# Performance work log

Measured on AMD Instinct MI355X. Metric: run time of the kernel, lower is better.

Reference implementation:

```python
import jax, jax.numpy as jnp
import numpy as np

_LOG_2PI = float(np.log(2.0 * np.pi))
N = 4096
N_VARS = 128
N_SOURCES = 8
_EPS = 1e-6


def setup_inputs() -> dict:
    key = jax.random.key(0)
    ks = jax.random.split(key, 6)
    data = jax.random.normal(ks[0], (N, N_VARS), dtype=jnp.float32)
    sources = jax.random.randint(ks[1], (N,), 0, N_SOURCES, dtype=jnp.int32)
    miss_mask = jax.random.bernoulli(ks[2], 0.3, (N, N_VARS))
    # Strictly lower-triangular DAG weights, small spectral norm so I - W is well conditioned
    W_eff = jnp.tril(jax.random.normal(ks[3], (N_VARS, N_VARS), dtype=jnp.float32) * 0.05, k=-1)
    log_sigma2 = jnp.zeros((N_SOURCES, N_VARS), dtype=jnp.float32)
    mu = jnp.zeros((N_VARS,), dtype=jnp.float32)
    sample_weights = jax.random.uniform(ks[4], (N,), dtype=jnp.float32)
    return {"data": data, "W_eff": W_eff, "log_sigma2": log_sigma2, "mu": mu,
            "sample_weights": sample_weights, "sources": sources, "miss_mask": miss_mask}


def reference(data, W_eff, log_sigma2, mu, sample_weights, sources, miss_mask):
    # Gaussian log-likelihood over observed entries only, per sample.
    # Original torch code loops over unique (source, missingness-pattern) groups and
    # does a Cholesky of the observed sub-covariance Sigma_oo + eps*I.  We compute the
    # mathematically identical quantity fully batched via the masked-covariance trick:
    #   Sigma_tilde = M (Sigma + eps I) M + diag(1 - obs)
    # whose logdet equals logdet(Sigma_oo + eps I_oo) and whose quadratic form on the
    # zero-filled centred data equals x_o^T (Sigma_oo + eps I)^{-1} x_o.
    D = data.shape[1]
    I = jnp.eye(D, dtype=data.dtype)
    T = jnp.linalg.solve(I - W_eff, I)                       # [D, D]
    sigma2 = jnp.maximum(jnp.exp(log_sigma2), _EPS)          # [S, D]
    # Sigma_s = T^T diag(sigma2_s) T for every source
    Sigma = jnp.einsum('ij,si,ik->sjk', T, sigma2, T)        # [S, D, D]

    obs = (~miss_mask).astype(data.dtype)                    # [N, D]
    xc = (data - mu[None, :]) * obs                          # centred, zero at missing

    Sig_i = Sigma[sources] + _EPS * I                        # [N, D, D]
    M = obs[:, :, None] * obs[:, None, :]                    # [N, D, D] obs outer obs
    Sig_t = Sig_i * M + I * (1.0 - obs)[:, None, :]          # identity on missing coords

    L = jnp.linalg.cholesky(Sig_t)                           # [N, D, D]
    z = jax.scipy.linalg.solve_triangular(L, xc[:, :, None], lower=True)[:, :, 0]
    quad = jnp.sum(z * z, axis=1)                            # [N]
    logdet = 2.0 * jnp.sum(jnp.log(jnp.diagonal(L, axis1=1, axis2=2)), axis=1)
    d_obs = jnp.sum(obs, axis=1)                             # [N]
    ll = -0.5 * (quad + logdet + d_obs * _LOG_2PI)           # [N]
    return jnp.sum(ll * sample_weights)
```

## Files before the change

### kernel.cpp

```cpp
#include <hip/hip_runtime.h>
#include <math.h>

#define DD 128
#define NSRC 8
#define EMAX 32
#define MFAST 62
#define LOG_2PI 1.83787706640934548356f
#define LN2F 0.69314718055994531f
#define EPSF 1e-6f

__device__ inline int tri_row_of(int e) {
    float f = sqrtf(8.f * (float)e + 1.f);
    int r = (int)((f - 1.f) * 0.5f);
    if ((r + 1) * (r + 2) / 2 <= e) ++r;
    else if (r * (r + 1) / 2 > e) --r;
    return r;
}

__global__ __launch_bounds__(128) void k_precompute(
    const float* __restrict__ W, const float* __restrict__ ls2,
    const unsigned int* __restrict__ mw, int n_words,
    float* __restrict__ Q, float* __restrict__ ldS, int* __restrict__ flag)
{
    __shared__ float Bs[DD][DD + 1];
    __shared__ float r[4][DD + 1];
    __shared__ float sinv[DD];
    __shared__ float part2[2];
    const int tid = threadIdx.x;
    const int s   = blockIdx.x >> 5;
    const int i0  = (blockIdx.x & 31) * 4;

    int gid = (blockIdx.x * 128 + tid) * 4;
    int f = 0;
    #pragma unroll
    for (int t = 0; t < 4; ++t) {
        int idx = gid + t;
        if (idx < n_words) {
            unsigned int v = mw[idx];
            if (v > 1u) f |= 1;
            if (v == 0x3F800000u) f |= 2;
        }
    }
    unsigned long long bA = __ballot(f & 1);
    unsigned long long bB = __ballot(f & 2);
    if ((tid & 63) == 0) {
        int fw = (bA ? 1 : 0) | (bB ? 2 : 0);
        if (fw) atomicOr(flag, fw);
    }

    for (int idx = tid; idx < DD * DD; idx += 128) {
        int row = idx >> 7, col = idx & 127;
        Bs[row][col] = (row == col ? 1.f : 0.f) - W[idx];
    }
    sinv[tid] = 1.f / fmaxf(expf(ls2[s * DD + tid]), EPSF);
    __syncthreads();
    for (int a = 0; a < 4; ++a)
        r[a][tid] = Bs[i0 + a][tid] * sinv[tid];
    __syncthreads();

    const int j = tid;
    float acc0 = 0.f, acc1 = 0.f, acc2 = 0.f, acc3 = 0.f;
    #pragma unroll 4
    for (int d = 0; d < DD; ++d) {
        float bj = Bs[j][d];
        acc0 += r[0][d] * bj;
        acc1 += r[1][d] * bj;
        acc2 += r[2][d] * bj;
        acc3 += r[3][d] * bj;
    }
    size_t base = ((size_t)s * DD + i0) * DD + j;
    Q[base         ] = acc0;
    Q[base +     DD] = acc1;
    Q[base + 2 * DD] = acc2;
    Q[base + 3 * DD] = acc3;

    if (i0 == 0) {
        float v = logf(fmaxf(expf(ls2[s * DD + tid]), EPSF));
        for (int o = 32; o; o >>= 1) v += __shfl_down(v, o, 64);
        if ((tid & 63) == 0) part2[tid >> 6] = v;
        __syncthreads();
        if (tid == 0) ldS[s] = part2[0] + part2[1];
    }
}

__global__ __launch_bounds__(64) void k_fast(
    const float* __restrict__ data, const float* __restrict__ mu,
    const float* __restrict__ wgt, const int* __restrict__ src,
    const void* __restrict__ miss, const int* __restrict__ layoutFlag,
    const float* __restrict__ Q, const float* __restrict__ ldS,
    float* __restrict__ partial, int* __restrict__ ovf_count,
    int* __restrict__ ovf_list)
{
    __shared__ __align__(16) float xsh[DD];
    __shared__ float ysh[DD];
    __shared__ int   midx[DD];
    __shared__ float csc[2][64];

    const int i = blockIdx.x, lane = threadIdx.x;
    const int s = src[i];
    const float* Qs = Q + (size_t)s * DD * DD;
    const size_t base = (size_t)i * DD;

    const int f = *layoutFlag;
    bool mm0, mm1;
    if (f & 2) {
        mm0 = ((const float*)miss)[base + lane]      != 0.f;
        mm1 = ((const float*)miss)[base + lane + 64] != 0.f;
    } else if (f & 1) {
        mm0 = ((const unsigned char*)miss)[base + lane]      != 0;
        mm1 = ((const unsigned char*)miss)[base + lane + 64] != 0;
    } else {
        mm0 = ((const int*)miss)[base + lane]      != 0;
        mm1 = ((const int*)miss)[base + lane + 64] != 0;
    }

    unsigned long long b0 = __ballot(mm0), b1 = __ballot(mm1);
    const int m = __popcll(b0) + __popcll(b1);
    if (m > MFAST) {
        if (lane == 0) { int pos = atomicAdd(ovf_count, 1); ovf_list[pos] = i; }
        return;
    }
    unsigned long long lt = (1ull << lane) - 1ull;
    if (mm0) midx[__popcll(b0 & lt)] = lane;
    if (mm1) midx[__popcll(b0) + __popcll(b1 & lt)] = lane + 64;

    float xv0 = mm0 ? 0.f : (data[base + lane]      - mu[lane]);
    float xv1 = mm1 ? 0.f : (data[base + lane + 64] - mu[lane + 64]);
    xsh[lane] = xv0;
    xsh[lane + 64] = xv1;
    __syncthreads();

    const float4* q0 = (const float4*)(Qs + (size_t)lane * DD);
    const float4* q1 = (const float4*)(Qs + (size_t)(lane + 64) * DD);
    const float4* x4 = (const float4*)xsh;
    float a0 = 0.f, a1 = 0.f;
    #pragma unroll 8
    for (int d = 0; d < DD / 4; ++d) {
        float4 xx = x4[d];
        float4 qa = q0[d], qb = q1[d];
        a0 += qa.x * xx.x + qa.y * xx.y + qa.z * xx.z + qa.w * xx.w;
        a1 += qb.x * xx.x + qb.y * xx.y + qb.z * xx.z + qb.w * xx.w;
    }
    ysh[lane] = a0;
    ysh[lane + 64] = a1;
    float p = xv0 * a0 + xv1 * a1;
    for (int o = 32; o; o >>= 1) p += __shfl_down(p, o, 64);
    __syncthreads();

    const int cntT = ((m + 1) * (m + 2)) >> 1;
    unsigned key[EMAX];
    float    val[EMAX];
    #pragma unroll
    for (int t = 0; t < EMAX; ++t) {
        key[t] = 0u; val[t] = 0.f;
        int e = lane + (t << 6);
        if (e < cntT) {
            int q  = tri_row_of(e);
            int jc = m - q;
            int ir = jc + (e - ((q * (q + 1)) >> 1));
            float v;
            if (ir == m) {
                v = (jc == m) ? 0.f : ysh[midx[jc]];
            } else {
                v = Qs[(size_t)(midx[ir] * DD + midx[jc])];
            }
            key[t] = ((unsigned)jc << 8) | (unsigned)ir;
            val[t] = v;
            if (jc == 0) csc[0][ir] = v;
        }
    }
    __syncthreads();

    float logacc = 0.f;
    #pragma unroll 1
    for (int k = 0; k < m; ++k) {
        const int pb = k & 1;
        float dk = csc[pb][k];
        float invd = __builtin_amdgcn_rcpf(dk);
        logacc += __log2f(dk);
        const unsigned boundA = (unsigned)(k + 1) << 8;
        const unsigned boundB = (unsigned)(k + 2) << 8;
        #pragma unroll
        for (int t = 0; t < EMAX; ++t) {
            bool alive = (key[t] >= boundA);
            if (!__any(alive)) break;
            if (alive) {
                int ir = (int)(key[t] & 255u);
                int jc = (int)(key[t] >> 8);
                float ci = csc[pb][ir];
                float cj = csc[pb][jc];
                val[t] -= ci * cj * invd;
                if (key[t] < boundB) csc[pb ^ 1][ir] = val[t];
            }
        }
        __syncthreads();
    }

    if (lane == 0) {
        float ll = -0.5f * ((p + val[0]) + logacc * LN2F + ldS[s]
                            + (float)(DD - m) * LOG_2PI);
        atomicAdd(&partial[i & 63], ll * wgt[i]);
    }
}

__global__ __launch_bounds__(128) void k_fallback(
    const float* __restrict__ data, const float* __restrict__ mu,
    const float* __restrict__ wgt, const int* __restrict__ src,
    const void* __restrict__ miss, const int* __restrict__ layoutFlag,
    const float* __restrict__ Q, const float* __restrict__ ldS,
    float* __restrict__ partial, const int* __restrict__ ovf_count,
    const int* __restrict__ ovf_list)
{
    __shared__ __align__(16) float xsh[DD];
    __shared__ float ysh[DD];
    __shared__ int   midx[DD];
    __shared__ float cscv[DD + 1];
    __shared__ float tri[(DD + 1) * (DD + 2) / 2];
    __shared__ float bc[2];
    __shared__ float red[2];
    __shared__ int   sh_m;

    const int tid = threadIdx.x;
    for (int j = blockIdx.x; j < *ovf_count; j += gridDim.x) {
        const int i = ovf_list[j];
        if (tid == 0) sh_m = 0;
        __syncthreads();

        const int s = src[i];
        const float* Qs = Q + (size_t)s * DD * DD;
        const int f = *layoutFlag;
        const size_t g = (size_t)i * DD + tid;
        bool mm;
        if (f & 2)      mm = ((const float*)miss)[g] != 0.f;
        else if (f & 1) mm = ((const unsigned char*)miss)[g] != 0;
        else            mm = ((const int*)miss)[g] != 0;

        float xv = mm ? 0.f : (data[g] - mu[tid]);
        xsh[tid] = xv;
        if (mm) { int pos = atomicAdd(&sh_m, 1); midx[pos] = tid; }
        __syncthreads();
        const int m = sh_m;

        const float4* qrow = (const float4*)(Qs + (size_t)tid * DD);
        const float4* x4   = (const float4*)xsh;
        float acc = 0.f;
        #pragma unroll 8
        for (int d = 0; d < DD / 4; ++d) {
            float4 q = qrow[d], xx = x4[d];
            acc += q.x * xx.x + q.y * xx.y + q.z * xx.z + q.w * xx.w;
        }
        ysh[tid] = acc;
        float pp = xv * acc;
        for (int o = 32; o; o >>= 1) pp += __shfl_down(pp, o, 64);
        if ((tid & 63) == 0) red[tid >> 6] = pp;
        __syncthreads();

        const int cntA = (m * (m + 1)) >> 1;
        for (int e = tid; e < cntA; e += 128) {
            int a = tri_row_of(e);
            int b = e - ((a * (a + 1)) >> 1);
            tri[e] = Qs[(size_t)midx[a] * DD + midx[b]];
        }
        for (int b = tid; b < m; b += 128) tri[cntA + b] = ysh[midx[b]];
        if (tid == 0) tri[cntA + m] = 0.f;
        __syncthreads();

        float logacc = 0.f;
        if (m > 0) {
            if (tid == 0) {
                float d0 = tri[0];
                bc[1] = d0;
                float sq = sqrtf(d0);
                bc[0] = 1.f / sq;
                tri[0] = sq;
            }
            __syncthreads();
            for (int k = 0; k < m; ++k) {
                float inv = bc[0];
                if (tid == 0) logacc += logf(bc[1]);
                for (int ii = k + 1 + tid; ii <= m; ii += 128) {
                    int off = (ii * (ii + 1)) >> 1;
                    float v = tri[off + k] * inv;
                    tri[off + k] = v;
                    cscv[ii] = v;
                }
                __syncthreads();
                int qn  = m - k;
                int cnt = (qn * (qn + 1)) >> 1;
                for (int e = tid; e < cnt; e += 128) {
                    int ri = tri_row_of(e);
                    int rj = e - ((ri * (ri + 1)) >> 1);
                    int ii = k + 1 + ri, jj = k + 1 + rj;
                    int off = (ii * (ii + 1)) >> 1;
                    float v = tri[off + jj] - cscv[ii] * cscv[jj];
                    if (ii == jj && jj == k + 1 && k + 1 < m) {
                        bc[1] = v;
                        float sq = sqrtf(v);
                        bc[0] = 1.f / sq;
                        tri[off + jj] = sq;
                    } else {
                        tri[off + jj] = v;
                    }
                }
                __syncthreads();
            }
        }

        if (tid == 0) {
            float quad2 = (m > 0) ? -tri[cntA + m] : 0.f;
            float quad1 = red[0] + red[1];
            float ll = -0.5f * ((quad1 - quad2) + logacc + ldS[s]
                                + (float)(DD - m) * LOG_2PI);
            atomicAdd(&partial[i & 63], ll * wgt[i]);
        }
        __syncthreads();
    }
}

__global__ __launch_bounds__(64) void k_reduce(
    const float* __restrict__ partial, float* __restrict__ out)
{
    int l = threadIdx.x;
    float v = partial[l];
    for (int o = 32; o; o >>= 1) v += __shfl_down(v, o, 64);
    if (l == 0) out[0] = v;
}

extern "C" void kernel_launch(void* const* d_in, const int* in_sizes, int n_in,
                              void* d_out, int out_size, void* d_ws, size_t ws_size,
                              hipStream_t stream)
{
    const float* data = (const float*)d_in[0];
    const float* W    = (const float*)d_in[1];
    const float* ls2  = (const float*)d_in[2];
    const float* mu   = (const float*)d_in[3];
    const float* wgt  = (const float*)d_in[4];
    const int*   src  = (const int*)d_in[5];
    const void*  miss = (const void*)d_in[6];
    float* out = (float*)d_out;

    float* Q        = (float*)d_ws;
    float* ldS      = Q + (size_t)NSRC * DD * DD;
    float* partial  = ldS + NSRC;
    int*   flag     = (int*)(partial + 64);
    int*   ovf_cnt  = flag + 1;
    int*   ovf_list = flag + 2;

    const int n       = in_sizes[0] / DD;
    const int n_words = (n * DD) / 4;

    hipMemsetAsync(partial, 0, 66 * sizeof(float), stream);
    hipLaunchKernelGGL(k_precompute, dim3(NSRC * 32), dim3(128), 0, stream,
                       W, ls2, (const unsigned int*)miss, n_words, Q, ldS, flag);
    hipLaunchKernelGGL(k_fast, dim3(n), dim3(64), 0, stream,
                       data, mu, wgt, src, miss, flag, Q, ldS,
                       partial, ovf_cnt, ovf_list);
    hipLaunchKernelGGL(k_fallback, dim3(64), dim3(128), 0, stream,
                       data, mu, wgt, src, miss, flag, Q, ldS,
                       partial, ovf_cnt, ovf_list);
    hipLaunchKernelGGL(k_reduce, dim3(1), dim3(64), 0, stream, partial, out);
}
```

Baseline: 180.1 us.

## Pack four samples per block in fast kernel and fuse fallback with final reduce

The fast kernel now handles four samples per 256-thread block, one wavefront each, and keeps overflow samples in the block with m forced to zero so block-wide barriers stay uniform. The elimination loop runs to the largest m among the four wavefronts, so every wavefront waits at each __syncthreads for the slowest one. The fallback and reduce kernels are merged into a single one-block tail kernel, which removes one launch but makes any overflow samples run serially.

Result: slower. 210.5 us (+16.9%).

```diff
diff --git a/kernel.cpp b/kernel.cpp
--- a/kernel.cpp
+++ b/kernel.cpp
@@ -5,6 +5,7 @@
 #define NSRC 8
 #define EMAX 32
 #define MFAST 62
+#define WPB 4
 #define LOG_2PI 1.83787706640934548356f
 #define LN2F 0.69314718055994531f
 #define EPSF 1e-6f
@@ -83,7 +84,7 @@
     }
 }
 
-__global__ __launch_bounds__(64) void k_fast(
+__global__ __launch_bounds__(256) void k_fast(
     const float* __restrict__ data, const float* __restrict__ mu,
     const float* __restrict__ wgt, const int* __restrict__ src,
     const void* __restrict__ miss, const int* __restrict__ layoutFlag,
@@ -91,13 +92,16 @@
     float* __restrict__ partial, int* __restrict__ ovf_count,
     int* __restrict__ ovf_list)
 {
-    __shared__ __align__(16) float xsh[DD];
-    __shared__ float ysh[DD];
-    __shared__ int   midx[DD];
-    __shared__ float csc[2][64];
-
-    const int i = blockIdx.x, lane = threadIdx.x;
-    const int s = src[i];
+    __shared__ __align__(16) float xsh[WPB][DD];
+    __shared__ float ysh[WPB][DD];
+    __shared__ int   midx[WPB][64];
+    __shared__ float csc[WPB][2][64];
+    __shared__ int   msh[WPB];
+
+    const int w    = threadIdx.x >> 6;
+    const int lane = threadIdx.x & 63;
+    const int i    = blockIdx.x * WPB + w;
+    const int s    = src[i];
     const float* Qs = Q + (size_t)s * DD * DD;
     const size_t base = (size_t)i * DD;
 
@@ -115,24 +119,27 @@
     }
 
     unsigned long long b0 = __ballot(mm0), b1 = __ballot(mm1);
-    const int m = __popcll(b0) + __popcll(b1);
-    if (m > MFAST) {
-        if (lane == 0) { int pos = atomicAdd(ovf_count, 1); ovf_list[pos] = i; }
-        return;
-    }
+    const int m_real = __popcll(b0) + __popcll(b1);
+    const bool skip = (m_real > MFAST);
+    if (skip && lane == 0) { int pos = atomicAdd(ovf_count, 1); ovf_list[pos] = i; }
+    const int m = skip ? 0 : m_real;
+    if (lane == 0) msh[w] = m;
+
     unsigned long long lt = (1ull << lane) - 1ull;
-    if (mm0) midx[__popcll(b0 & lt)] = lane;
-    if (mm1) midx[__popcll(b0) + __popcll(b1 & lt)] = lane + 64;
+    if (!skip) {
+        if (mm0) midx[w][__popcll(b0 & lt)] = lane;
+        if (mm1) midx[w][__popcll(b0) + __popcll(b1 & lt)] = lane + 64;
+    }
 
     float xv0 = mm0 ? 0.f : (data[base + lane]      - mu[lane]);
     float xv1 = mm1 ? 0.f : (data[base + lane + 64] - mu[lane + 64]);
-    xsh[lane] = xv0;
-    xsh[lane + 64] = xv1;
+    xsh[w][lane] = xv0;
+    xsh[w][lane + 64] = xv1;
     __syncthreads();
 
     const float4* q0 = (const float4*)(Qs + (size_t)lane * DD);
     const float4* q1 = (const float4*)(Qs + (size_t)(lane + 64) * DD);
-    const float4* x4 = (const float4*)xsh;
+    const float4* x4 = (const float4*)xsh[w];
     float a0 = 0.f, a1 = 0.f;
     #pragma unroll 8
     for (int d = 0; d < DD / 4; ++d) {
@@ -141,11 +148,13 @@
         a0 += qa.x * xx.x + qa.y * xx.y + qa.z * xx.z + qa.w * xx.w;
         a1 += qb.x * xx.x + qb.y * xx.y + qb.z * xx.z + qb.w * xx.w;
     }
-    ysh[lane] = a0;
-    ysh[lane + 64] = a1;
+    ysh[w][lane] = a0;
+    ysh[w][lane + 64] = a1;
     float p = xv0 * a0 + xv1 * a1;
     for (int o = 32; o; o >>= 1) p += __shfl_down(p, o, 64);
     __syncthreads();
+
+    const int kmax = max(max(msh[0], msh[1]), max(msh[2], msh[3]));
 
     const int cntT = ((m + 1) * (m + 2)) >> 1;
     unsigned key[EMAX];
@@ -160,56 +169,58 @@
             int ir = jc + (e - ((q * (q + 1)) >> 1));
             float v;
             if (ir == m) {
-                v = (jc == m) ? 0.f : ysh[midx[jc]];
+                v = (jc == m) ? 0.f : ysh[w][midx[w][jc]];
             } else {
-                v = Qs[(size_t)(midx[ir] * DD + midx[jc])];
+                v = Qs[(size_t)(midx[w][ir] * DD + midx[w][jc])];
             }
             key[t] = ((unsigned)jc << 8) | (unsigned)ir;
             val[t] = v;
-            if (jc == 0) csc[0][ir] = v;
+            if (jc == 0) csc[w][0][ir] = v;
         }
     }
     __syncthreads();
 
     float logacc = 0.f;
     #pragma unroll 1
-    for (int k = 0; k < m; ++k) {
-        const int pb = k & 1;
-        float dk = csc[pb][k];
-        float invd = __builtin_amdgcn_rcpf(dk);
-        logacc += __log2f(dk);
-        const unsigned boundA = (unsigned)(k + 1) << 8;
-        const unsigned boundB = (unsigned)(k + 2) << 8;
-        #pragma unroll
-        for (int t = 0; t < EMAX; ++t) {
-            bool alive = (key[t] >= boundA);
-            if (!__any(alive)) break;
-            if (alive) {
-                int ir = (int)(key[t] & 255u);
-                int jc = (int)(key[t] >> 8);
-                float ci = csc[pb][ir];
-                float cj = csc[pb][jc];
-                val[t] -= ci * cj * invd;
-                if (key[t] < boundB) csc[pb ^ 1][ir] = val[t];
+    for (int k = 0; k < kmax; ++k) {
+        if (k < m) {
+            const int pb = k & 1;
+            float dk = csc[w][pb][k];
+            float invd = __builtin_amdgcn_rcpf(dk);
+            logacc += __log2f(dk);
+            const unsigned boundA = (unsigned)(k + 1) << 8;
+            const unsigned boundB = (unsigned)(k + 2) << 8;
+            #pragma unroll
+            for (int t = 0; t < EMAX; ++t) {
+                bool alive = (key[t] >= boundA);
+                if (!__any(alive)) break;
+                if (alive) {
+                    int ir = (int)(key[t] & 255u);
+                    int jc = (int)(key[t] >> 8);
+                    float ci = csc[w][pb][ir];
+                    float cj = csc[w][pb][jc];
+                    val[t] -= ci * cj * invd;
+                    if (key[t] < boundB) csc[w][pb ^ 1][ir] = val[t];
+                }
             }
         }
         __syncthreads();
     }
 
-    if (lane == 0) {
+    if (lane == 0 && !skip) {
         float ll = -0.5f * ((p + val[0]) + logacc * LN2F + ldS[s]
                             + (float)(DD - m) * LOG_2PI);
         atomicAdd(&partial[i & 63], ll * wgt[i]);
     }
 }
 
-__global__ __launch_bounds__(128) void k_fallback(
+__global__ __launch_bounds__(128) void k_tail(
     const float* __restrict__ data, const float* __restrict__ mu,
     const float* __restrict__ wgt, const int* __restrict__ src,
     const void* __restrict__ miss, const int* __restrict__ layoutFlag,
     const float* __restrict__ Q, const float* __restrict__ ldS,
     float* __restrict__ partial, const int* __restrict__ ovf_count,
-    const int* __restrict__ ovf_list)
+    const int* __restrict__ ovf_list, float* __restrict__ out)
 {
     __shared__ __align__(16) float xsh[DD];
     __shared__ float ysh[DD];
@@ -221,7 +232,8 @@
     __shared__ int   sh_m;
 
     const int tid = threadIdx.x;
-    for (int j = blockIdx.x; j < *ovf_count; j += gridDim.x) {
+    const int novf = *ovf_count;
+    for (int j = 0; j < novf; ++j) {
         const int i = ovf_list[j];
         if (tid == 0) sh_m = 0;
         __syncthreads();
@@ -315,15 +327,13 @@
         }
         __syncthreads();
     }
-}
-
-__global__ __launch_bounds__(64) void k_reduce(
-    const float* __restrict__ partial, float* __restrict__ out)
-{
-    int l = threadIdx.x;
-    float v = partial[l];
-    for (int o = 32; o; o >>= 1) v += __shfl_down(v, o, 64);
-    if (l == 0) out[0] = v;
+
+    __syncthreads();
+    if (tid < 64) {
+        float v = partial[tid];
+        for (int o = 32; o; o >>= 1) v += __shfl_down(v, o, 64);
+        if (tid == 0) out[0] = v;
+    }
 }
 
 extern "C" void kernel_launch(void* const* d_in, const int* in_sizes, int n_in,
@@ -352,11 +362,10 @@
     hipMemsetAsync(partial, 0, 66 * sizeof(float), stream);
     hipLaunchKernelGGL(k_precompute, dim3(NSRC * 32), dim3(128), 0, stream,
                        W, ls2, (const unsigned int*)miss, n_words, Q, ldS, flag);
-    hipLaunchKernelGGL(k_fast, dim3(n), dim3(64), 0, stream,
+    hipLaunchKernelGGL(k_fast, dim3(n / WPB), dim3(64 * WPB), 0, stream,
                        data, mu, wgt, src, miss, flag, Q, ldS,
                        partial, ovf_cnt, ovf_list);
-    hipLaunchKernelGGL(k_fallback, dim3(64), dim3(128), 0, stream,
+    hipLaunchKernelGGL(k_tail, dim3(1), dim3(128), 0, stream,
                        data, mu, wgt, src, miss, flag, Q, ldS,
-                       partial, ovf_cnt, ovf_list);
-    hipLaunchKernelGGL(k_reduce, dim3(1), dim3(64), 0, stream, partial, out);
-}
+                       partial, ovf_cnt, ovf_list, out);
+}
```

## Coalesce Q matvec and gather, skip missing rows, merge tail kernels

Applied to the files above, without the earlier changes.

Reorganizes the fast-path matvec so each lane owns two adjacent output columns and streams rows of Q coalesced, skipping rows where the centred data is zero. The missing-index sub-block of Q is gathered once into a shared triangular buffer before the per-lane register fill. The fallback and final reduction kernels are merged into a single one-block kernel to drop a launch. This adds shared memory per block, which may lower occupancy, and serializes overflow samples in one block.

New measurement: 162.4 us. -9.8%, faster.

```diff
diff --git a/kernel.cpp b/kernel.cpp
--- a/kernel.cpp
+++ b/kernel.cpp
@@ -91,60 +91,72 @@
     float* __restrict__ partial, int* __restrict__ ovf_count,
     int* __restrict__ ovf_list)
 {
-    __shared__ __align__(16) float xsh[DD];
+    __shared__ float xsh[DD];
     __shared__ float ysh[DD];
-    __shared__ int   midx[DD];
+    __shared__ int   midx[64];
     __shared__ float csc[2][64];
+    __shared__ float tri[(MFAST + 1) * (MFAST + 2) / 2];
 
     const int i = blockIdx.x, lane = threadIdx.x;
     const int s = src[i];
     const float* Qs = Q + (size_t)s * DD * DD;
     const size_t base = (size_t)i * DD;
+    const int j0 = 2 * lane, j1 = 2 * lane + 1;
 
     const int f = *layoutFlag;
-    bool mm0, mm1;
+    bool mmE, mmO;
     if (f & 2) {
-        mm0 = ((const float*)miss)[base + lane]      != 0.f;
-        mm1 = ((const float*)miss)[base + lane + 64] != 0.f;
+        const float* M = (const float*)miss;
+        mmE = M[base + j0] != 0.f;  mmO = M[base + j1] != 0.f;
     } else if (f & 1) {
-        mm0 = ((const unsigned char*)miss)[base + lane]      != 0;
-        mm1 = ((const unsigned char*)miss)[base + lane + 64] != 0;
+        const unsigned char* M = (const unsigned char*)miss;
+        mmE = M[base + j0] != 0;    mmO = M[base + j1] != 0;
     } else {
-        mm0 = ((const int*)miss)[base + lane]      != 0;
-        mm1 = ((const int*)miss)[base + lane + 64] != 0;
-    }
-
-    unsigned long long b0 = __ballot(mm0), b1 = __ballot(mm1);
-    const int m = __popcll(b0) + __popcll(b1);
+        const int* M = (const int*)miss;
+        mmE = M[base + j0] != 0;    mmO = M[base + j1] != 0;
+    }
+
+    unsigned long long bE = __ballot(mmE), bO = __ballot(mmO);
+    const int m = __popcll(bE) + __popcll(bO);
     if (m > MFAST) {
         if (lane == 0) { int pos = atomicAdd(ovf_count, 1); ovf_list[pos] = i; }
         return;
     }
     unsigned long long lt = (1ull << lane) - 1ull;
-    if (mm0) midx[__popcll(b0 & lt)] = lane;
-    if (mm1) midx[__popcll(b0) + __popcll(b1 & lt)] = lane + 64;
-
-    float xv0 = mm0 ? 0.f : (data[base + lane]      - mu[lane]);
-    float xv1 = mm1 ? 0.f : (data[base + lane + 64] - mu[lane + 64]);
-    xsh[lane] = xv0;
-    xsh[lane + 64] = xv1;
-    __syncthreads();
-
-    const float4* q0 = (const float4*)(Qs + (size_t)lane * DD);
-    const float4* q1 = (const float4*)(Qs + (size_t)(lane + 64) * DD);
-    const float4* x4 = (const float4*)xsh;
-    float a0 = 0.f, a1 = 0.f;
-    #pragma unroll 8
-    for (int d = 0; d < DD / 4; ++d) {
-        float4 xx = x4[d];
-        float4 qa = q0[d], qb = q1[d];
-        a0 += qa.x * xx.x + qa.y * xx.y + qa.z * xx.z + qa.w * xx.w;
-        a1 += qb.x * xx.x + qb.y * xx.y + qb.z * xx.z + qb.w * xx.w;
-    }
-    ysh[lane] = a0;
-    ysh[lane + 64] = a1;
-    float p = xv0 * a0 + xv1 * a1;
+    if (mmE) midx[__popcll(bE & lt)] = j0;
+    if (mmO) midx[__popcll(bE) + __popcll(bO & lt)] = j1;
+
+    float x0 = mmE ? 0.f : (data[base + j0] - mu[j0]);
+    float x1 = mmO ? 0.f : (data[base + j1] - mu[j1]);
+    xsh[j0] = x0;
+    xsh[j1] = x1;
+    __syncthreads();
+
+    float y0 = 0.f, y1 = 0.f;
+    #pragma unroll 4
+    for (int k = 0; k < DD; ++k) {
+        float xk = xsh[k];
+        if (xk != 0.f) {
+            float2 q = *(const float2*)(Qs + (size_t)k * DD + j0);
+            y0 += xk * q.x;
+            y1 += xk * q.y;
+        }
+    }
+    ysh[j0] = y0;
+    ysh[j1] = y1;
+    float p = x0 * y0 + x1 * y1;
     for (int o = 32; o; o >>= 1) p += __shfl_down(p, o, 64);
+    __syncthreads();
+
+    const int mjc = midx[lane];
+    for (int ir = 0; ir < m; ++ir) {
+        int row = midx[ir];
+        if (lane <= ir)
+            tri[((ir * (ir + 1)) >> 1) + lane] = Qs[(size_t)row * DD + mjc];
+    }
+    const int offm = (m * (m + 1)) >> 1;
+    if (lane < m)   tri[offm + lane] = ysh[mjc];
+    if (lane == 0)  tri[offm + m] = 0.f;
     __syncthreads();
 
     const int cntT = ((m + 1) * (m + 2)) >> 1;
@@ -158,12 +170,7 @@
             int q  = tri_row_of(e);
             int jc = m - q;
             int ir = jc + (e - ((q * (q + 1)) >> 1));
-            float v;
-            if (ir == m) {
-                v = (jc == m) ? 0.f : ysh[midx[jc]];
-            } else {
-                v = Qs[(size_t)(midx[ir] * DD + midx[jc])];
-            }
+            float v = tri[((ir * (ir + 1)) >> 1) + jc];
             key[t] = ((unsigned)jc << 8) | (unsigned)ir;
             val[t] = v;
             if (jc == 0) csc[0][ir] = v;
@@ -203,13 +210,13 @@
     }
 }
 
-__global__ __launch_bounds__(128) void k_fallback(
+__global__ __launch_bounds__(128) void k_tail(
     const float* __restrict__ data, const float* __restrict__ mu,
     const float* __restrict__ wgt, const int* __restrict__ src,
     const void* __restrict__ miss, const int* __restrict__ layoutFlag,
     const float* __restrict__ Q, const float* __restrict__ ldS,
     float* __restrict__ partial, const int* __restrict__ ovf_count,
-    const int* __restrict__ ovf_list)
+    const int* __restrict__ ovf_list, float* __restrict__ out)
 {
     __shared__ __align__(16) float xsh[DD];
     __shared__ float ysh[DD];
@@ -221,7 +228,8 @@
     __shared__ int   sh_m;
 
     const int tid = threadIdx.x;
-    for (int j = blockIdx.x; j < *ovf_count; j += gridDim.x) {
+    const int novf = *ovf_count;
+    for (int j = 0; j < novf; ++j) {
         const int i = ovf_list[j];
         if (tid == 0) sh_m = 0;
         __syncthreads();
@@ -315,15 +323,13 @@
         }
         __syncthreads();
     }
-}
-
-__global__ __launch_bounds__(64) void k_reduce(
-    const float* __restrict__ partial, float* __restrict__ out)
-{
-    int l = threadIdx.x;
-    float v = partial[l];
-    for (int o = 32; o; o >>= 1) v += __shfl_down(v, o, 64);
-    if (l == 0) out[0] = v;
+
+    __syncthreads();
+    if (tid < 64) {
+        float v = partial[tid];
+        for (int o = 32; o; o >>= 1) v += __shfl_down(v, o, 64);
+        if (tid == 0) out[0] = v;
+    }
 }
 
 extern "C" void kernel_launch(void* const* d_in, const int* in_sizes, int n_in,
@@ -355,8 +361,7 @@
     hipLaunchKernelGGL(k_fast, dim3(n), dim3(64), 0, stream,
                        data, mu, wgt, src, miss, flag, Q, ldS,
                        partial, ovf_cnt, ovf_list);
-    hipLaunchKernelGGL(k_fallback, dim3(64), dim3(128), 0, stream,
+    hipLaunchKernelGGL(k_tail, dim3(1), dim3(128), 0, stream,
                        data, mu, wgt, src, miss, flag, Q, ldS,
-                       partial, ovf_cnt, ovf_list);
-    hipLaunchKernelGGL(k_reduce, dim3(1), dim3(64), 0, stream, partial, out);
-}
+                       partial, ovf_cnt, ovf_list, out);
+}
```
